# Performance work log

Measured on AMD Instinct MI355X. Metric: run time of the kernel, lower is better.

The kernel has to match this reference:

```python
import jax, jax.numpy as jnp
import numpy as np

NUM_SRC1, NUM_DST1 = 2_000_000, 131_072
NUM_SRC2, NUM_DST2 = 131_072, 8_192
E1, E2 = NUM_DST1 * 15, NUM_DST2 * 15
F_IN, F_H = 128, 128


def setup_inputs() -> dict:
    key = jax.random.key(0)
    ks = jax.random.split(key, 10)
    return {
        "x": jax.random.normal(ks[0], (NUM_SRC1, F_IN), dtype=jnp.float32),
        "edge1_src": jax.random.randint(ks[1], (E1,), 0, NUM_SRC1, dtype=jnp.int32),
        "edge1_dst": jax.random.randint(ks[2], (E1,), 0, NUM_DST1, dtype=jnp.int32),
        "edge2_src": jax.random.randint(ks[3], (E2,), 0, NUM_SRC2, dtype=jnp.int32),
        "edge2_dst": jax.random.randint(ks[4], (E2,), 0, NUM_DST2, dtype=jnp.int32),
        "num_dst1": NUM_DST1,
        "num_dst2": NUM_DST2,
        "W_self1": jax.random.normal(ks[5], (F_IN, F_H), dtype=jnp.float32) * 0.05,
        "W_neigh1": jax.random.normal(ks[6], (F_IN, F_H), dtype=jnp.float32) * 0.05,
        "b1": jnp.zeros((F_H,), dtype=jnp.float32),
        "W_self2": jax.random.normal(ks[7], (F_H, F_H), dtype=jnp.float32) * 0.05,
        "W_neigh2": jax.random.normal(ks[8], (F_H, F_H), dtype=jnp.float32) * 0.05,
        "b2": jnp.zeros((F_H,), dtype=jnp.float32),
    }


def _sage_mean(h_src, h_dst, e_src, e_dst, num_dst, W_self, W_neigh, b):
    # mean-aggregate neighbor feats per dst, then linear transforms (DGL SAGEConv, aggr='mean')
    agg = jax.ops.segment_sum(h_src[e_src], e_dst, num_segments=num_dst)  # [num_dst, F]
    deg = jax.ops.segment_sum(jnp.ones((e_dst.shape[0],), h_src.dtype), e_dst,
                              num_segments=num_dst)
    mean = agg / jnp.maximum(deg, 1.0)[:, None]
    return h_dst @ W_self + mean @ W_neigh + b


def reference(x, edge1_src, edge1_dst, edge2_src, edge2_dst, num_dst1, num_dst2,
              W_self1, W_neigh1, b1, W_self2, W_neigh2, b2):
    h_dst = x[:num_dst1]
    h = _sage_mean(x, h_dst, edge1_src, edge1_dst, num_dst1, W_self1, W_neigh1, b1)
    h = jax.nn.relu(h)
    h_dst2 = h[:num_dst2]
    out = _sage_mean(h, h_dst2, edge2_src, edge2_dst, num_dst2, W_self2, W_neigh2, b2)
    return out
```

## Files before the change

kernel.cpp:

```cpp
#include <hip/hip_runtime.h>

static constexpr int FDIM = 128;
static constexpr int ND1  = 131072;
static constexpr int ND2  = 8192;
static constexpr int LDP  = 56;

using bf16x8 = __attribute__((ext_vector_type(8))) short;
using u16x8  = __attribute__((ext_vector_type(8))) unsigned short;
using f32x4  = __attribute__((ext_vector_type(4))) float;

static __device__ __forceinline__ unsigned short f2bf(float f) {
  unsigned u = __float_as_uint(f);
  u = (u + 0x7FFFu + ((u >> 16) & 1u)) >> 16;
  return (unsigned short)u;
}
static __device__ __forceinline__ float bf2f(unsigned short s) {
  return __uint_as_float(((unsigned)s) << 16);
}

__global__ void hist_all(const int* __restrict__ e1d, const int* __restrict__ e2d,
                         int* __restrict__ rs1, int* __restrict__ rs2, int E1, int E2) {
  const int n1 = E1 >> 2, n2 = E2 >> 2;
  int t = blockIdx.x * 256 + threadIdx.x;
  if (t < n1) {
    int4 d = ((const int4*)e1d)[t];
    atomicAdd(&rs1[d.x], 1); atomicAdd(&rs1[d.y], 1);
    atomicAdd(&rs1[d.z], 1); atomicAdd(&rs1[d.w], 1);
  } else if (t < n1 + n2) {
    int4 d = ((const int4*)e2d)[t - n1];
    atomicAdd(&rs2[d.x], 1); atomicAdd(&rs2[d.y], 1);
    atomicAdd(&rs2[d.z], 1); atomicAdd(&rs2[d.w], 1);
  }
  if (blockIdx.x == 0) {
    int tt = threadIdx.x;
    if (tt < (E1 & 3)) atomicAdd(&rs1[e1d[E1 - 1 - tt]], 1);
    int t2 = tt - 8;
    if (t2 >= 0 && t2 < (E2 & 3)) atomicAdd(&rs2[e2d[E2 - 1 - t2]], 1);
  }
}

__global__ __launch_bounds__(1024) void scan2_kernel(int* __restrict__ c1, int n1,
                                                     int* __restrict__ c2, int n2) {
  int* c = blockIdx.x ? c2 : c1;
  const int n = blockIdx.x ? n2 : n1;
  const int tid = threadIdx.x;
  const int chunk = n >> 10;
  const int base = tid * chunk;
  int s = 0;
  for (int j = 0; j < chunk; j += 4) {
    int4 v = *(const int4*)&c[base + j];
    s += v.x + v.y + v.z + v.w;
  }
  __shared__ int ps[1024];
  ps[tid] = s;
  __syncthreads();
  for (int off = 1; off < 1024; off <<= 1) {
    int v = (tid >= off) ? ps[tid - off] : 0;
    __syncthreads();
    ps[tid] += v;
    __syncthreads();
  }
  int run = (tid == 0) ? 0 : ps[tid - 1];
  for (int j = 0; j < chunk; j += 4) {
    int4 v = *(const int4*)&c[base + j];
    int4 o;
    o.x = run; run += v.x; o.y = run; run += v.y;
    o.z = run; run += v.z; o.w = run; run += v.w;
    *(int4*)&c[base + j] = o;
  }
  if (tid == 1023) c[n] = run;
}

__global__ void fill_all(const int* __restrict__ e1s, const int* __restrict__ e1d,
                         const int* __restrict__ e2s, const int* __restrict__ e2d,
                         const int* __restrict__ rs1, const int* __restrict__ rs2,
                         int* __restrict__ cur1, int* __restrict__ cur2,
                         int* __restrict__ csr1, int* __restrict__ csr2, int E1, int E2) {
  const int n1 = E1 >> 2, n2 = E2 >> 2;
  int t = blockIdx.x * 256 + threadIdx.x;
  if (t < n1) {
    int4 d = ((const int4*)e1d)[t];
    int4 s = ((const int4*)e1s)[t];
    int p;
    p = atomicAdd(&cur1[d.x], 1); csr1[rs1[d.x] + p] = s.x;
    p = atomicAdd(&cur1[d.y], 1); csr1[rs1[d.y] + p] = s.y;
    p = atomicAdd(&cur1[d.z], 1); csr1[rs1[d.z] + p] = s.z;
    p = atomicAdd(&cur1[d.w], 1); csr1[rs1[d.w] + p] = s.w;
  } else if (t < n1 + n2) {
    int4 d = ((const int4*)e2d)[t - n1];
    int4 s = ((const int4*)e2s)[t - n1];
    int p;
    p = atomicAdd(&cur2[d.x], 1); csr2[rs2[d.x] + p] = s.x;
    p = atomicAdd(&cur2[d.y], 1); csr2[rs2[d.y] + p] = s.y;
    p = atomicAdd(&cur2[d.z], 1); csr2[rs2[d.z] + p] = s.z;
    p = atomicAdd(&cur2[d.w], 1); csr2[rs2[d.w] + p] = s.w;
  }
  if (blockIdx.x == 0) {
    int tt = threadIdx.x;
    if (tt < (E1 & 3)) {
      int e = E1 - 1 - tt, d = e1d[e];
      int p = atomicAdd(&cur1[d], 1); csr1[rs1[d] + p] = e1s[e];
    }
    int t2 = tt - 8;
    if (t2 >= 0 && t2 < (E2 & 3)) {
      int e = E2 - 1 - t2, d = e2d[e];
      int p = atomicAdd(&cur2[d], 1); csr2[rs2[d] + p] = e2s[e];
    }
  }
}

__global__ void prep_w(const float* __restrict__ Ws1, const float* __restrict__ Wn1,
                       unsigned short* __restrict__ Wt1,
                       const float* __restrict__ Ws2, const float* __restrict__ Wn2,
                       unsigned short* __restrict__ Wt2) {
  int t = blockIdx.x * 256 + threadIdx.x;
  int which = t >> 15;
  int r = t & 32767;
  int col = r >> 8, k = r & 255;
  const float* Ws = which ? Ws2 : Ws1;
  const float* Wn = which ? Wn2 : Wn1;
  unsigned short* Wt = which ? Wt2 : Wt1;
  float v = (k < 128) ? Ws[k * 128 + col] : Wn[(k - 128) * 128 + col];
  Wt[col * 256 + k] = f2bf(v);
}

__global__ __launch_bounds__(256)
void gather_mean1(const float* __restrict__ src, const int* __restrict__ csr,
                  const int* __restrict__ rs, unsigned short* __restrict__ out, int nrows) {
  const int lane = threadIdx.x & 63;
  const int half = lane >> 5;
  const int sub  = lane & 31;
  int row = (int)((blockIdx.x * (unsigned)blockDim.x + threadIdx.x) >> 6);
  row = __builtin_amdgcn_readfirstlane(row);
  if (row >= nrows) return;
  const int start = rs[row], end = rs[row + 1];
  float ax = 0.f, ay = 0.f, az = 0.f, aw = 0.f;
  for (int i = start; i < end; i += 16) {
    const int endm1 = end - 1;
    int cc[16];
    #pragma unroll
    for (int j = 0; j < 16; ++j) { int t = i + j; cc[j] = csr[t < endm1 ? t : endm1]; }
    float4 v[8];
    #pragma unroll
    for (int j = 0; j < 8; ++j) {
      int e = half ? cc[2 * j + 1] : cc[2 * j];
      v[j] = *(const float4*)(src + (size_t)e * FDIM + sub * 4);
    }
    #pragma unroll
    for (int j = 0; j < 8; ++j) {
      float mk = (i + 2 * j + half) < end ? 1.f : 0.f;
      ax = fmaf(v[j].x, mk, ax); ay = fmaf(v[j].y, mk, ay);
      az = fmaf(v[j].z, mk, az); aw = fmaf(v[j].w, mk, aw);
    }
  }
  ax += __shfl_xor(ax, 32); ay += __shfl_xor(ay, 32);
  az += __shfl_xor(az, 32); aw += __shfl_xor(aw, 32);
  if (half == 0) {
    const int deg = end - start;
    const float inv = 1.f / (float)(deg > 1 ? deg : 1);
    ushort4 o;
    o.x = f2bf(ax * inv); o.y = f2bf(ay * inv);
    o.z = f2bf(az * inv); o.w = f2bf(aw * inv);
    *(ushort4*)(out + (size_t)row * FDIM + sub * 4) = o;
  }
}

__global__ __launch_bounds__(256)
void gather_mean2(const unsigned short* __restrict__ src, const int* __restrict__ csr,
                  const int* __restrict__ rs, unsigned short* __restrict__ out, int nrows) {
  const int lane = threadIdx.x & 63;
  const int half = lane >> 5;
  const int sub  = lane & 31;
  int row = (int)((blockIdx.x * (unsigned)blockDim.x + threadIdx.x) >> 6);
  row = __builtin_amdgcn_readfirstlane(row);
  if (row >= nrows) return;
  const int start = rs[row], end = rs[row + 1];
  float ax = 0.f, ay = 0.f, az = 0.f, aw = 0.f;
  for (int i = start; i < end; i += 16) {
    const int endm1 = end - 1;
    int cc[16];
    #pragma unroll
    for (int j = 0; j < 16; ++j) { int t = i + j; cc[j] = csr[t < endm1 ? t : endm1]; }
    ushort4 v[8];
    #pragma unroll
    for (int j = 0; j < 8; ++j) {
      int e = half ? cc[2 * j + 1] : cc[2 * j];
      v[j] = *(const ushort4*)(src + (size_t)e * FDIM + sub * 4);
    }
    #pragma unroll
    for (int j = 0; j < 8; ++j) {
      float mk = (i + 2 * j + half) < end ? 1.f : 0.f;
      ax = fmaf(bf2f(v[j].x), mk, ax); ay = fmaf(bf2f(v[j].y), mk, ay);
      az = fmaf(bf2f(v[j].z), mk, az); aw = fmaf(bf2f(v[j].w), mk, aw);
    }
  }
  ax += __shfl_xor(ax, 32); ay += __shfl_xor(ay, 32);
  az += __shfl_xor(az, 32); aw += __shfl_xor(aw, 32);
  if (half == 0) {
    const int deg = end - start;
    const float inv = 1.f / (float)(deg > 1 ? deg : 1);
    ushort4 o;
    o.x = f2bf(ax * inv); o.y = f2bf(ay * inv);
    o.z = f2bf(az * inv); o.w = f2bf(aw * inv);
    *(ushort4*)(out + (size_t)row * FDIM + sub * 4) = o;
  }
}

template<bool RELU, bool AX_BF16, bool OUT_F32>
__global__ __launch_bounds__(256)
void gemm_mfma(const void* __restrict__ Axp,
               const unsigned short* __restrict__ Am,
               const unsigned short* __restrict__ Wt,
               const float* __restrict__ bias,
               void* __restrict__ Outp) {
  __shared__ unsigned short Asb[128 * LDP];
  __shared__ unsigned short Wsb[128 * LDP];
  const int tid  = threadIdx.x;
  const int lane = tid & 63;
  const int w    = tid >> 6;
  const int row0 = blockIdx.x * 128;
  const int p    = lane & 15;
  const int q    = lane >> 4;

  f32x4 acc[2][8];
  #pragma unroll
  for (int m = 0; m < 2; ++m)
    #pragma unroll
    for (int n = 0; n < 8; ++n) acc[m][n] = (f32x4){0.f, 0.f, 0.f, 0.f};

  const int sr = tid >> 1;
  const int sk = (tid & 1) * 16;

  for (int c = 0; c < 8; ++c) {
    const int kc = c * 32;
    const int kl = kc & 127;
    {
      const unsigned short* wsrc = Wt + (size_t)sr * 256 + kc + sk;
      u16x8 a = *(const u16x8*)(wsrc);
      u16x8 b = *(const u16x8*)(wsrc + 8);
      *(u16x8*)&Wsb[sr * LDP + sk]     = a;
      *(u16x8*)&Wsb[sr * LDP + sk + 8] = b;
    }
    if (AX_BF16 || c >= 4) {
      const unsigned short* asrc =
          (c < 4 ? (const unsigned short*)Axp : Am) + (size_t)(row0 + sr) * FDIM + kl + sk;
      u16x8 a = *(const u16x8*)(asrc);
      u16x8 b = *(const u16x8*)(asrc + 8);
      *(u16x8*)&Asb[sr * LDP + sk]     = a;
      *(u16x8*)&Asb[sr * LDP + sk + 8] = b;
    } else {
      const float* asrc = (const float*)Axp + (size_t)(row0 + sr) * FDIM + kl + sk;
      float4 f0 = *(const float4*)(asrc);
      float4 f1 = *(const float4*)(asrc + 4);
      float4 f2 = *(const float4*)(asrc + 8);
      float4 f3 = *(const float4*)(asrc + 12);
      u16x8 a, b;
      a[0] = f2bf(f0.x); a[1] = f2bf(f0.y); a[2] = f2bf(f0.z); a[3] = f2bf(f0.w);
      a[4] = f2bf(f1.x); a[5] = f2bf(f1.y); a[6] = f2bf(f1.z); a[7] = f2bf(f1.w);
      b[0] = f2bf(f2.x); b[1] = f2bf(f2.y); b[2] = f2bf(f2.z); b[3] = f2bf(f2.w);
      b[4] = f2bf(f3.x); b[5] = f2bf(f3.y); b[6] = f2bf(f3.z); b[7] = f2bf(f3.w);
      *(u16x8*)&Asb[sr * LDP + sk]     = a;
      *(u16x8*)&Asb[sr * LDP + sk + 8] = b;
    }
    __syncthreads();
    bf16x8 af[2];
    #pragma unroll
    for (int m = 0; m < 2; ++m)
      af[m] = *(const bf16x8*)&Asb[(w * 32 + m * 16 + p) * LDP + q * 8];
    #pragma unroll
    for (int n = 0; n < 8; ++n) {
      bf16x8 bfr = *(const bf16x8*)&Wsb[(n * 16 + p) * LDP + q * 8];
      acc[0][n] = __builtin_amdgcn_mfma_f32_16x16x32_bf16(af[0], bfr, acc[0][n], 0, 0, 0);
      acc[1][n] = __builtin_amdgcn_mfma_f32_16x16x32_bf16(af[1], bfr, acc[1][n], 0, 0, 0);
    }
    __syncthreads();
  }

  #pragma unroll
  for (int n = 0; n < 8; ++n) {
    const int col = n * 16 + p;
    const float bv = bias[col];
    #pragma unroll
    for (int m = 0; m < 2; ++m) {
      #pragma unroll
      for (int r = 0; r < 4; ++r) {
        float y = acc[m][n][r] + bv;
        if (RELU) y = fmaxf(y, 0.f);
        const size_t grow = (size_t)(row0 + w * 32 + m * 16 + q * 4 + r);
        if (OUT_F32) ((float*)Outp)[grow * FDIM + col] = y;
        else         ((unsigned short*)Outp)[grow * FDIM + col] = f2bf(y);
      }
    }
  }
}

extern "C" void kernel_launch(void* const* d_in, const int* in_sizes, int n_in,
                              void* d_out, int out_size, void* d_ws, size_t ws_size,
                              hipStream_t stream) {
  const float* x   = (const float*)d_in[0];
  const int*   e1s = (const int*)d_in[1];
  const int*   e1d = (const int*)d_in[2];
  const int*   e2s = (const int*)d_in[3];
  const int*   e2d = (const int*)d_in[4];
  const float* Ws1 = (const float*)d_in[7];
  const float* Wn1 = (const float*)d_in[8];
  const float* b1  = (const float*)d_in[9];
  const float* Ws2 = (const float*)d_in[10];
  const float* Wn2 = (const float*)d_in[11];
  const float* b2  = (const float*)d_in[12];
  const int E1 = in_sizes[1];
  const int E2 = in_sizes[3];

  char* pw = (char*)d_ws;
  unsigned short* agg1 = (unsigned short*)pw; pw += (size_t)ND1 * FDIM * 2;
  unsigned short* h    = (unsigned short*)pw; pw += (size_t)ND1 * FDIM * 2;
  unsigned short* agg2 = (unsigned short*)pw; pw += (size_t)ND2 * FDIM * 2;
  unsigned short* Wt1  = (unsigned short*)pw; pw += (size_t)FDIM * 256 * 2;
  unsigned short* Wt2  = (unsigned short*)pw; pw += (size_t)FDIM * 256 * 2;
  int* csr1 = (int*)pw; pw += (size_t)E1 * 4;
  int* csr2 = (int*)pw; pw += (size_t)E2 * 4;
  int* rs1  = (int*)pw; pw += (size_t)(ND1 + 4) * 4;
  int* rs2  = (int*)pw; pw += (size_t)(ND2 + 4) * 4;
  int* cur1 = (int*)pw; pw += (size_t)ND1 * 4;
  int* cur2 = (int*)pw; pw += (size_t)ND2 * 4;
  const size_t ZB = (size_t)(ND1 + 4 + ND2 + 4 + ND1 + ND2) * 4;

  hipMemsetAsync(rs1, 0, ZB, stream);
  prep_w<<<256, 256, 0, stream>>>(Ws1, Wn1, Wt1, Ws2, Wn2, Wt2);

  const int n4 = (E1 >> 2) + (E2 >> 2);
  hist_all<<<(n4 + 255) / 256, 256, 0, stream>>>(e1d, e2d, rs1, rs2, E1, E2);
  scan2_kernel<<<2, 1024, 0, stream>>>(rs1, ND1, rs2, ND2);
  fill_all<<<(n4 + 255) / 256, 256, 0, stream>>>(e1s, e1d, e2s, e2d, rs1, rs2,
                                                 cur1, cur2, csr1, csr2, E1, E2);

  gather_mean1<<<ND1 / 4, 256, 0, stream>>>(x, csr1, rs1, agg1, ND1);
  gemm_mfma<true, false, false><<<ND1 / 128, 256, 0, stream>>>(x, agg1, Wt1, b1, h);

  gather_mean2<<<ND2 / 4, 256, 0, stream>>>(h, csr2, rs2, agg2, ND2);
  gemm_mfma<false, true, true><<<ND2 / 128, 256, 0, stream>>>(h, agg2, Wt2, b2, (float*)d_out);
}
```

Before: 499.6 us.

## Assign one row per half-wave in gathers and fold weight prep into histogram

The gather kernels now map one destination row to each 32-lane half-wave instead of a full wave. Each half-wave loads up to 32 neighbor indices cooperatively and broadcasts them with shuffles, which removes the redundant per-lane index loads and the cross-half reduction. The grid shrinks by half to match. The weight-transpose kernel is merged into the histogram launch as extra blocks, saving one kernel launch. Row-wise divergence between the two halves of a wave may cost some efficiency because degrees vary.

Measured after the change: 479.1 us. 4.1% less time.

```diff
diff --git a/kernel.cpp b/kernel.cpp
--- a/kernel.cpp
+++ b/kernel.cpp
@@ -18,8 +18,24 @@
   return __uint_as_float(((unsigned)s) << 16);
 }
 
-__global__ void hist_all(const int* __restrict__ e1d, const int* __restrict__ e2d,
-                         int* __restrict__ rs1, int* __restrict__ rs2, int E1, int E2) {
+__global__ void build_hist(const int* __restrict__ e1d, const int* __restrict__ e2d,
+                           int* __restrict__ rs1, int* __restrict__ rs2, int E1, int E2,
+                           const float* __restrict__ Ws1, const float* __restrict__ Wn1,
+                           unsigned short* __restrict__ Wt1,
+                           const float* __restrict__ Ws2, const float* __restrict__ Wn2,
+                           unsigned short* __restrict__ Wt2, int nb_hist) {
+  if ((int)blockIdx.x >= nb_hist) {
+    int t = (blockIdx.x - nb_hist) * 256 + threadIdx.x;
+    int which = t >> 15;
+    int r = t & 32767;
+    int col = r >> 8, k = r & 255;
+    const float* Ws = which ? Ws2 : Ws1;
+    const float* Wn = which ? Wn2 : Wn1;
+    unsigned short* Wt = which ? Wt2 : Wt1;
+    float v = (k < 128) ? Ws[k * 128 + col] : Wn[(k - 128) * 128 + col];
+    Wt[col * 256 + k] = f2bf(v);
+    return;
+  }
   const int n1 = E1 >> 2, n2 = E2 >> 2;
   int t = blockIdx.x * 256 + threadIdx.x;
   if (t < n1) {
@@ -109,101 +125,82 @@
   }
 }
 
-__global__ void prep_w(const float* __restrict__ Ws1, const float* __restrict__ Wn1,
-                       unsigned short* __restrict__ Wt1,
-                       const float* __restrict__ Ws2, const float* __restrict__ Wn2,
-                       unsigned short* __restrict__ Wt2) {
-  int t = blockIdx.x * 256 + threadIdx.x;
-  int which = t >> 15;
-  int r = t & 32767;
-  int col = r >> 8, k = r & 255;
-  const float* Ws = which ? Ws2 : Ws1;
-  const float* Wn = which ? Wn2 : Wn1;
-  unsigned short* Wt = which ? Wt2 : Wt1;
-  float v = (k < 128) ? Ws[k * 128 + col] : Wn[(k - 128) * 128 + col];
-  Wt[col * 256 + k] = f2bf(v);
-}
-
 __global__ __launch_bounds__(256)
 void gather_mean1(const float* __restrict__ src, const int* __restrict__ csr,
                   const int* __restrict__ rs, unsigned short* __restrict__ out, int nrows) {
-  const int lane = threadIdx.x & 63;
+  const int tid  = threadIdx.x;
+  const int lane = tid & 63;
   const int half = lane >> 5;
   const int sub  = lane & 31;
-  int row = (int)((blockIdx.x * (unsigned)blockDim.x + threadIdx.x) >> 6);
-  row = __builtin_amdgcn_readfirstlane(row);
+  const int wid  = (int)((blockIdx.x * 256u + tid) >> 6);
+  const int row  = wid * 2 + half;
   if (row >= nrows) return;
-  const int start = rs[row], end = rs[row + 1];
+  const int start = rs[row];
+  const int deg   = rs[row + 1] - start;
   float ax = 0.f, ay = 0.f, az = 0.f, aw = 0.f;
-  for (int i = start; i < end; i += 16) {
-    const int endm1 = end - 1;
-    int cc[16];
-    #pragma unroll
-    for (int j = 0; j < 16; ++j) { int t = i + j; cc[j] = csr[t < endm1 ? t : endm1]; }
-    float4 v[8];
-    #pragma unroll
-    for (int j = 0; j < 8; ++j) {
-      int e = half ? cc[2 * j + 1] : cc[2 * j];
-      v[j] = *(const float4*)(src + (size_t)e * FDIM + sub * 4);
-    }
-    #pragma unroll
-    for (int j = 0; j < 8; ++j) {
-      float mk = (i + 2 * j + half) < end ? 1.f : 0.f;
-      ax = fmaf(v[j].x, mk, ax); ay = fmaf(v[j].y, mk, ay);
-      az = fmaf(v[j].z, mk, az); aw = fmaf(v[j].w, mk, aw);
-    }
-  }
-  ax += __shfl_xor(ax, 32); ay += __shfl_xor(ay, 32);
-  az += __shfl_xor(az, 32); aw += __shfl_xor(aw, 32);
-  if (half == 0) {
-    const int deg = end - start;
-    const float inv = 1.f / (float)(deg > 1 ? deg : 1);
-    ushort4 o;
-    o.x = f2bf(ax * inv); o.y = f2bf(ay * inv);
-    o.z = f2bf(az * inv); o.w = f2bf(aw * inv);
-    *(ushort4*)(out + (size_t)row * FDIM + sub * 4) = o;
-  }
+  for (int base = 0; base < deg; base += 32) {
+    int t = base + sub;
+    int idx = csr[start + (t < deg ? t : deg - 1)];
+    const int lim = (deg - base) < 32 ? (deg - base) : 32;
+    for (int b = 0; b < lim; b += 8) {
+      float4 v[8];
+      #pragma unroll
+      for (int j = 0; j < 8; ++j) {
+        int e = __shfl(idx, half * 32 + b + j);
+        v[j] = *(const float4*)(src + (size_t)e * FDIM + sub * 4);
+      }
+      #pragma unroll
+      for (int j = 0; j < 8; ++j) {
+        float mk = (b + j) < lim ? 1.f : 0.f;
+        ax = fmaf(v[j].x, mk, ax); ay = fmaf(v[j].y, mk, ay);
+        az = fmaf(v[j].z, mk, az); aw = fmaf(v[j].w, mk, aw);
+      }
+    }
+  }
+  const float inv = 1.f / (float)(deg > 1 ? deg : 1);
+  ushort4 o;
+  o.x = f2bf(ax * inv); o.y = f2bf(ay * inv);
+  o.z = f2bf(az * inv); o.w = f2bf(aw * inv);
+  *(ushort4*)(out + (size_t)row * FDIM + sub * 4) = o;
 }
 
 __global__ __launch_bounds__(256)
 void gather_mean2(const unsigned short* __restrict__ src, const int* __restrict__ csr,
                   const int* __restrict__ rs, unsigned short* __restrict__ out, int nrows) {
-  const int lane = threadIdx.x & 63;
+  const int tid  = threadIdx.x;
+  const int lane = tid & 63;
   const int half = lane >> 5;
   const int sub  = lane & 31;
-  int row = (int)((blockIdx.x * (unsigned)blockDim.x + threadIdx.x) >> 6);
-  row = __builtin_amdgcn_readfirstlane(row);
+  const int wid  = (int)((blockIdx.x * 256u + tid) >> 6);
+  const int row  = wid * 2 + half;
   if (row >= nrows) return;
-  const int start = rs[row], end = rs[row + 1];
+  const int start = rs[row];
+  const int deg   = rs[row + 1] - start;
   float ax = 0.f, ay = 0.f, az = 0.f, aw = 0.f;
-  for (int i = start; i < end; i += 16) {
-    const int endm1 = end - 1;
-    int cc[16];
-    #pragma unroll
-    for (int j = 0; j < 16; ++j) { int t = i + j; cc[j] = csr[t < endm1 ? t : endm1]; }
-    ushort4 v[8];
-    #pragma unroll
-    for (int j = 0; j < 8; ++j) {
-      int e = half ? cc[2 * j + 1] : cc[2 * j];
-      v[j] = *(const ushort4*)(src + (size_t)e * FDIM + sub * 4);
-    }
-    #pragma unroll
-    for (int j = 0; j < 8; ++j) {
-      float mk = (i + 2 * j + half) < end ? 1.f : 0.f;
-      ax = fmaf(bf2f(v[j].x), mk, ax); ay = fmaf(bf2f(v[j].y), mk, ay);
-      az = fmaf(bf2f(v[j].z), mk, az); aw = fmaf(bf2f(v[j].w), mk, aw);
-    }
-  }
-  ax += __shfl_xor(ax, 32); ay += __shfl_xor(ay, 32);
-  az += __shfl_xor(az, 32); aw += __shfl_xor(aw, 32);
-  if (half == 0) {
-    const int deg = end - start;
-    const float inv = 1.f / (float)(deg > 1 ? deg : 1);
-    ushort4 o;
-    o.x = f2bf(ax * inv); o.y = f2bf(ay * inv);
-    o.z = f2bf(az * inv); o.w = f2bf(aw * inv);
-    *(ushort4*)(out + (size_t)row * FDIM + sub * 4) = o;
-  }
+  for (int base = 0; base < deg; base += 32) {
+    int t = base + sub;
+    int idx = csr[start + (t < deg ? t : deg - 1)];
+    const int lim = (deg - base) < 32 ? (deg - base) : 32;
+    for (int b = 0; b < lim; b += 8) {
+      ushort4 v[8];
+      #pragma unroll
+      for (int j = 0; j < 8; ++j) {
+        int e = __shfl(idx, half * 32 + b + j);
+        v[j] = *(const ushort4*)(src + (size_t)e * FDIM + sub * 4);
+      }
+      #pragma unroll
+      for (int j = 0; j < 8; ++j) {
+        float mk = (b + j) < lim ? 1.f : 0.f;
+        ax = fmaf(bf2f(v[j].x), mk, ax); ay = fmaf(bf2f(v[j].y), mk, ay);
+        az = fmaf(bf2f(v[j].z), mk, az); aw = fmaf(bf2f(v[j].w), mk, aw);
+      }
+    }
+  }
+  const float inv = 1.f / (float)(deg > 1 ? deg : 1);
+  ushort4 o;
+  o.x = f2bf(ax * inv); o.y = f2bf(ay * inv);
+  o.z = f2bf(az * inv); o.w = f2bf(aw * inv);
+  *(ushort4*)(out + (size_t)row * FDIM + sub * 4) = o;
 }
 
 template<bool RELU, bool AX_BF16, bool OUT_F32>
@@ -326,17 +323,18 @@
   const size_t ZB = (size_t)(ND1 + 4 + ND2 + 4 + ND1 + ND2) * 4;
 
   hipMemsetAsync(rs1, 0, ZB, stream);
-  prep_w<<<256, 256, 0, stream>>>(Ws1, Wn1, Wt1, Ws2, Wn2, Wt2);
 
   const int n4 = (E1 >> 2) + (E2 >> 2);
-  hist_all<<<(n4 + 255) / 256, 256, 0, stream>>>(e1d, e2d, rs1, rs2, E1, E2);
+  const int nb_hist = (n4 + 255) / 256;
+  build_hist<<<nb_hist + 256, 256, 0, stream>>>(e1d, e2d, rs1, rs2, E1, E2,
+                                                Ws1, Wn1, Wt1, Ws2, Wn2, Wt2, nb_hist);
   scan2_kernel<<<2, 1024, 0, stream>>>(rs1, ND1, rs2, ND2);
   fill_all<<<(n4 + 255) / 256, 256, 0, stream>>>(e1s, e1d, e2s, e2d, rs1, rs2,
                                                  cur1, cur2, csr1, csr2, E1, E2);
 
-  gather_mean1<<<ND1 / 4, 256, 0, stream>>>(x, csr1, rs1, agg1, ND1);
+  gather_mean1<<<ND1 / 8, 256, 0, stream>>>(x, csr1, rs1, agg1, ND1);
   gemm_mfma<true, false, false><<<ND1 / 128, 256, 0, stream>>>(x, agg1, Wt1, b1, h);
 
-  gather_mean2<<<ND2 / 4, 256, 0, stream>>>(h, csr2, rs2, agg2, ND2);
+  gather_mean2<<<ND2 / 8, 256, 0, stream>>>(h, csr2, rs2, agg2, ND2);
   gemm_mfma<false, true, true><<<ND2 / 128, 256, 0, stream>>>(h, agg2, Wt2, b2, (float*)d_out);
 }
```
